# Performance work log

Measured on AMD Instinct MI355X. Metric: run time of the kernel, lower is better.

## Reference

```python
import jax, jax.numpy as jnp
import numpy as np


def setup_inputs() -> dict:
    key = jax.random.key(0)
    ks = jax.random.split(key, 6)
    B, S, D, U = 32, 2048, 1024, 1024
    scale = 1.0 / np.sqrt(D)
    return {
        "h_enc": jax.random.normal(ks[0], (B, S, D), dtype=jnp.float32),
        "h_dec": jax.random.normal(ks[1], (B, D), dtype=jnp.float32),
        "W_enc": jax.random.normal(ks[2], (D, U), dtype=jnp.float32) * scale,
        "b_enc": jnp.zeros((U,), dtype=jnp.float32),
        "W_dec": jax.random.normal(ks[3], (D, U), dtype=jnp.float32) * scale,
        "b_dec": jnp.zeros((U,), dtype=jnp.float32),
        "W_com": jax.random.normal(ks[4], (U, 1), dtype=jnp.float32) * (1.0 / np.sqrt(U)),
        "b_com": jnp.zeros((1,), dtype=jnp.float32),
    }


def reference(h_enc, h_dec, W_enc, b_enc, W_dec, b_dec, W_com, b_com):
    # h_enc: [B,S,D] -> projected enc features [B,S,U]
    enc_p = jnp.einsum("bsd,du->bsu", h_enc, W_enc) + b_enc
    # h_dec: [B,D] -> [B,1,U]
    dec_p = (h_dec @ W_dec + b_dec)[:, None, :]
    # additive score: [B,S,1]
    score = jnp.einsum("bsu,uo->bso", jnp.tanh(dec_p + enc_p), W_com) + b_com
    attn = jax.nn.softmax(score, axis=1)  # softmax over seq axis
    # NOTE: original code multiplies attn by the PROJECTED h_enc (reassigned)
    context_vec = jnp.sum(attn * enc_p, axis=1)  # [B,U]
    return (context_vec, attn)
```

## Files before the change

### kernel.cpp

```cpp
#include <hip/hip_runtime.h>
#include <math.h>
#include <stdint.h>

#define Bz 32
#define Sz 2048
#define Dz 1024
#define Uz 1024
#define Mz (Bz*Sz)

typedef __attribute__((ext_vector_type(8))) short bf16x8;
typedef __attribute__((ext_vector_type(4))) float f32x4;

__device__ __forceinline__ unsigned short f2bf(float f) {
    union { float f; uint32_t u; } v; v.f = f;
    uint32_t r = v.u + 0x7FFFu + ((v.u >> 16) & 1u);
    return (unsigned short)(r >> 16);
}

__device__ __forceinline__ float fast_tanh(float x) {
    float e = __expf(2.f * x);
    return 1.f - 2.f * __builtin_amdgcn_rcpf(e + 1.f);
}

#define GLD16(gsrc, ldst) \
    __builtin_amdgcn_global_load_lds((__attribute__((address_space(1))) void*)(void*)(gsrc), \
        (__attribute__((address_space(3))) void*)(ldst), 16, 0, 0)

#define CONV_BLOCKS 16384
#define WT_BLOCKS   256
#define DECI_BLOCKS 32
#define SINIT_BLOCKS 64

__global__ __launch_bounds__(256) void prep_kernel(
    const float* __restrict__ h_enc, unsigned short* __restrict__ hbf,
    const float* __restrict__ W_enc, unsigned short* __restrict__ wT,
    const float* __restrict__ b_dec, float* __restrict__ dec_p,
    const float* __restrict__ b_com, float* __restrict__ score)
{
    __shared__ float tile[64][65];
    const int bid = blockIdx.x;
    const int tid = threadIdx.x;
    if (bid < CONV_BLOCKS) {
        const size_t i = ((size_t)bid * 256 + tid) * 16;
#pragma unroll
        for (int h = 0; h < 2; ++h) {
            const float4 a = *(const float4*)(h_enc + i + h * 8);
            const float4 c = *(const float4*)(h_enc + i + h * 8 + 4);
            union { unsigned short s[8]; uint4 v; } o;
            o.s[0] = f2bf(a.x); o.s[1] = f2bf(a.y); o.s[2] = f2bf(a.z); o.s[3] = f2bf(a.w);
            o.s[4] = f2bf(c.x); o.s[5] = f2bf(c.y); o.s[6] = f2bf(c.z); o.s[7] = f2bf(c.w);
            *(uint4*)(hbf + i + h * 8) = o.v;
        }
    } else if (bid < CONV_BLOCKS + WT_BLOCKS) {
        const int b2 = bid - CONV_BLOCKS;
        const int c  = tid & 63;
        const int r0 = tid >> 6;
        const int u0 = (b2 & 15) * 64;
        const int d0 = (b2 >> 4) * 64;
        for (int r = r0; r < 64; r += 4)
            tile[r][c] = W_enc[(size_t)(d0 + r) * Uz + u0 + c];
        __syncthreads();
        for (int r = r0; r < 64; r += 4)
            wT[(size_t)(u0 + r) * Dz + d0 + c] = f2bf(tile[c][r]);
    } else if (bid < CONV_BLOCKS + WT_BLOCKS + DECI_BLOCKS) {
        const int b3 = bid - (CONV_BLOCKS + WT_BLOCKS);
        const int u4 = tid * 4;
        *(float4*)&dec_p[b3 * Uz + u4] = *(const float4*)&b_dec[u4];
    } else {
        const int b4 = bid - (CONV_BLOCKS + WT_BLOCKS + DECI_BLOCKS);
        const float bc = b_com[0];
        const int i4 = (b4 * 256 + tid) * 4;
        float4 v = {bc, bc, bc, bc};
        *(float4*)&score[i4] = v;
    }
}

__global__ __launch_bounds__(256) void dec_partial_kernel(
    const float* __restrict__ h_dec, const float* __restrict__ W_dec,
    float* __restrict__ dec_p)
{
    __shared__ float hs[128];
    const int b  = blockIdx.x >> 3;
    const int d0 = (blockIdx.x & 7) * 128;
    const int tid = threadIdx.x;
    const int u4 = tid * 4;
    if (tid < 128) hs[tid] = h_dec[b * Dz + d0 + tid];
    __syncthreads();
    float4 acc = {0.f, 0.f, 0.f, 0.f};
#pragma unroll 4
    for (int d = 0; d < 128; ++d) {
        const float  a = hs[d];
        const float4 w = *(const float4*)&W_dec[(size_t)(d0 + d) * Uz + u4];
        acc.x += a * w.x; acc.y += a * w.y; acc.z += a * w.z; acc.w += a * w.w;
    }
    float* o = dec_p + b * Uz + u4;
    atomicAdd(o + 0, acc.x); atomicAdd(o + 1, acc.y);
    atomicAdd(o + 2, acc.z); atomicAdd(o + 3, acc.w);
}

__global__ __launch_bounds__(512, 2) void score_mfma_kernel(
    const unsigned short* __restrict__ hbf,
    const unsigned short* __restrict__ wT,
    const float* __restrict__ dec_p,
    const float* __restrict__ W_com,
    float* __restrict__ score)
{
    __shared__ unsigned short As[2][32 * 512];
    __shared__ unsigned short Bs[2][32 * 512];
    __shared__ float sred[4][256];

    const int tid  = threadIdx.x;
    const int w    = tid >> 6;
    const int lane = tid & 63;
    const int ln   = lane & 15;
    const int q    = lane >> 4;
    const int wm   = w >> 2;
    const int wn   = w & 3;

    const int xcd = blockIdx.x & 7;
    const int idx = blockIdx.x >> 3;
    const int mb  = xcd * 32 + (idx >> 2);
    const int m0  = mb * 256;
    const int ub  = (idx & 3) * 256;
    const int b   = m0 / Sz;

    const unsigned short* aA0 = hbf + (size_t)(m0 + w * 32 + ln) * Dz + q * 8;
    const unsigned short* aA1 = aA0 + (size_t)16 * Dz;
    const unsigned short* bB0 = wT + (size_t)(ub + w * 32 + ln) * Dz + q * 8;
    const unsigned short* bB1 = bB0 + (size_t)16 * Dz;

#define STAGE(nb_, k0_) do { \
        unsigned short* ad = &As[nb_][(w * 4) * 512]; \
        unsigned short* bd = &Bs[nb_][(w * 4) * 512]; \
        GLD16(aA0 + (k0_),      ad); \
        GLD16(aA0 + (k0_) + 32, ad + 512); \
        GLD16(aA1 + (k0_),      ad + 1024); \
        GLD16(aA1 + (k0_) + 32, ad + 1536); \
        GLD16(bB0 + (k0_),      bd); \
        GLD16(bB0 + (k0_) + 32, bd + 512); \
        GLD16(bB1 + (k0_),      bd + 1024); \
        GLD16(bB1 + (k0_) + 32, bd + 1536); \
    } while (0)

    f32x4 acc[8][4];
#pragma unroll
    for (int i = 0; i < 8; ++i)
#pragma unroll
        for (int j = 0; j < 4; ++j) acc[i][j] = (f32x4){0.f, 0.f, 0.f, 0.f};

#define COMPUTE(cb_) do { \
        _Pragma("unroll") \
        for (int kh = 0; kh < 2; ++kh) { \
            bf16x8 af[8], bfr[4]; \
            _Pragma("unroll") \
            for (int i = 0; i < 8; ++i) \
                af[i] = *(const bf16x8*)(&As[cb_][(((wm * 8 + i) << 1) + kh) * 512 + lane * 8]); \
            _Pragma("unroll") \
            for (int j = 0; j < 4; ++j) \
                bfr[j] = *(const bf16x8*)(&Bs[cb_][(((wn * 4 + j) << 1) + kh) * 512 + lane * 8]); \
            _Pragma("unroll") \
            for (int i = 0; i < 8; ++i) \
                _Pragma("unroll") \
                for (int j = 0; j < 4; ++j) \
                    acc[i][j] = __builtin_amdgcn_mfma_f32_16x16x32_bf16( \
                        af[i], bfr[j], acc[i][j], 0, 0, 0); \
        } \
    } while (0)

    STAGE(0, 0);
    __syncthreads();

    int nb = 0;
    for (int t = 0; t < 15; ++t) {
        STAGE(nb ^ 1, (t + 1) * 64);
        COMPUTE(nb);
        __syncthreads();
        nb ^= 1;
    }
    COMPUTE(nb);

    float dpv[4], wcv[4];
#pragma unroll
    for (int j = 0; j < 4; ++j) {
        const int u = ub + wn * 64 + j * 16 + ln;
        dpv[j] = dec_p[b * Uz + u];
        wcv[j] = W_com[u];
    }
    float racc[8][4];
#pragma unroll
    for (int i = 0; i < 8; ++i)
#pragma unroll
        for (int r = 0; r < 4; ++r) {
            float v = 0.f;
#pragma unroll
            for (int j = 0; j < 4; ++j)
                v += fast_tanh(acc[i][j][r] + dpv[j]) * wcv[j];
            racc[i][r] = v;
        }
#pragma unroll
    for (int off = 1; off < 16; off <<= 1)
#pragma unroll
        for (int i = 0; i < 8; ++i)
#pragma unroll
            for (int r = 0; r < 4; ++r)
                racc[i][r] += __shfl_xor(racc[i][r], off, 64);
    if (ln == 0) {
#pragma unroll
        for (int i = 0; i < 8; ++i)
#pragma unroll
            for (int r = 0; r < 4; ++r)
                sred[wn][wm * 128 + i * 16 + q * 4 + r] = racc[i][r];
    }
    __syncthreads();
    if (tid < 256) {
        const float s = sred[0][tid] + sred[1][tid] + sred[2][tid] + sred[3][tid];
        atomicAdd(&score[m0 + tid], s);
    }
#undef STAGE
#undef COMPUTE
}

__global__ __launch_bounds__(256) void softmax_init_kernel(
    const float* __restrict__ score, float* __restrict__ attn,
    const float* __restrict__ b_enc, float* __restrict__ out_ctx,
    float* __restrict__ wsum)
{
    __shared__ float red[256];
    const int tid = threadIdx.x;
    if (blockIdx.x >= 2 * Bz) {
        const int b3 = blockIdx.x - 2 * Bz;
        float4 z = {0.f, 0.f, 0.f, 0.f};
        *(float4*)&wsum[b3 * Dz + tid * 4] = z;
        return;
    }
    if (blockIdx.x >= Bz) {
        const int b2 = blockIdx.x - Bz;
        const int u4 = tid * 4;
        *(float4*)&out_ctx[b2 * Uz + u4] = *(const float4*)&b_enc[u4];
        return;
    }
    const int b = blockIdx.x;
    const float* srow = score + b * Sz;
    float v[8];
    float lm = -1e30f;
#pragma unroll
    for (int i = 0; i < 8; ++i) { v[i] = srow[i * 256 + tid]; lm = fmaxf(lm, v[i]); }
    red[tid] = lm; __syncthreads();
    for (int off = 128; off > 0; off >>= 1) {
        if (tid < off) red[tid] = fmaxf(red[tid], red[tid + off]);
        __syncthreads();
    }
    const float mx = red[0];
    __syncthreads();
    float ls = 0.f;
#pragma unroll
    for (int i = 0; i < 8; ++i) { v[i] = expf(v[i] - mx); ls += v[i]; }
    red[tid] = ls; __syncthreads();
    for (int off = 128; off > 0; off >>= 1) {
        if (tid < off) red[tid] += red[tid + off];
        __syncthreads();
    }
    const float inv = 1.f / red[0];
#pragma unroll
    for (int i = 0; i < 8; ++i) attn[b * Sz + i * 256 + tid] = v[i] * inv;
}

__global__ __launch_bounds__(256) void wsum_kernel(
    const float* __restrict__ h_enc, const float* __restrict__ attn,
    float* __restrict__ wsum)
{
    __shared__ float aw[64];
    const int b  = blockIdx.x >> 5;
    const int s0 = (blockIdx.x & 31) * 64;
    const int tid = threadIdx.x;
    if (tid < 64) aw[tid] = attn[b * Sz + s0 + tid];
    __syncthreads();
    float4 acc = {0.f, 0.f, 0.f, 0.f};
    const float* base = h_enc + ((size_t)b * Sz + s0) * Dz + tid * 4;
#pragma unroll 4
    for (int s = 0; s < 64; ++s) {
        const float a = aw[s];
        const float4 h = *(const float4*)(base + (size_t)s * Dz);
        acc.x += a * h.x; acc.y += a * h.y; acc.z += a * h.z; acc.w += a * h.w;
    }
    float* o = wsum + b * Dz + tid * 4;
    atomicAdd(o + 0, acc.x); atomicAdd(o + 1, acc.y);
    atomicAdd(o + 2, acc.z); atomicAdd(o + 3, acc.w);
}

__global__ __launch_bounds__(256) void ctx_partial_kernel(
    const float* __restrict__ wsum, const float* __restrict__ W_enc,
    float* __restrict__ out_ctx)
{
    __shared__ float hs[128];
    const int b  = blockIdx.x >> 3;
    const int d0 = (blockIdx.x & 7) * 128;
    const int tid = threadIdx.x;
    const int u4 = tid * 4;
    if (tid < 128) hs[tid] = wsum[b * Dz + d0 + tid];
    __syncthreads();
    float4 acc = {0.f, 0.f, 0.f, 0.f};
#pragma unroll 4
    for (int d = 0; d < 128; ++d) {
        const float  a = hs[d];
        const float4 wv = *(const float4*)&W_enc[(size_t)(d0 + d) * Uz + u4];
        acc.x += a * wv.x; acc.y += a * wv.y; acc.z += a * wv.z; acc.w += a * wv.w;
    }
    float* o = out_ctx + b * Uz + u4;
    atomicAdd(o + 0, acc.x); atomicAdd(o + 1, acc.y);
    atomicAdd(o + 2, acc.z); atomicAdd(o + 3, acc.w);
}

__global__ __launch_bounds__(256) void dec_proj_kernel(
    const float* __restrict__ h_dec, const float* __restrict__ W_dec,
    const float* __restrict__ b_dec, float* __restrict__ dec_p)
{
    __shared__ float hs[Dz];
    const int b = blockIdx.x >> 2;
    const int u = ((blockIdx.x & 3) << 8) + threadIdx.x;
    for (int d = threadIdx.x; d < Dz; d += 256) hs[d] = h_dec[b * Dz + d];
    __syncthreads();
    float acc = 0.f;
#pragma unroll 4
    for (int d = 0; d < Dz; ++d) acc += hs[d] * W_dec[d * Uz + u];
    dec_p[b * Uz + u] = acc + b_dec[u];
}

#define MT 64
#define NT 64
#define KT 64
__global__ __launch_bounds__(256) void score_kernel(
    const float* __restrict__ h_enc, const float* __restrict__ W_enc,
    const float* __restrict__ dec_p, const float* __restrict__ W_com,
    const float* __restrict__ b_com, float* __restrict__ score)
{
    __shared__ __align__(16) float As[KT][MT + 4];
    __shared__ __align__(16) float Bs[KT][NT + 4];
    __shared__ float red[MT][17];
    const int tid = threadIdx.x;
    const int tx = tid & 15;
    const int ty = tid >> 4;
    const int m0 = blockIdx.x * MT;
    const int b  = m0 / Sz;
    float s_acc = 0.f;
    for (int u0 = 0; u0 < Uz; u0 += NT) {
        float acc[4][4];
#pragma unroll
        for (int i = 0; i < 4; ++i)
#pragma unroll
            for (int j = 0; j < 4; ++j) acc[i][j] = 0.f;
        for (int k0 = 0; k0 < Dz; k0 += KT) {
            __syncthreads();
#pragma unroll
            for (int i = 0; i < 4; ++i) {
                const int row = ty + i * 16;
                const int c4  = tx * 4;
                const float4 v = *(const float4*)&h_enc[(size_t)(m0 + row) * Dz + k0 + c4];
                As[c4 + 0][row] = v.x; As[c4 + 1][row] = v.y;
                As[c4 + 2][row] = v.z; As[c4 + 3][row] = v.w;
            }
#pragma unroll
            for (int i = 0; i < 4; ++i) {
                const int row = ty + i * 16;
                *(float4*)&Bs[row][tx * 4] =
                    *(const float4*)&W_enc[(size_t)(k0 + row) * Uz + u0 + tx * 4];
            }
            __syncthreads();
#pragma unroll 8
            for (int k = 0; k < KT; ++k) {
                const float4 a = *(const float4*)&As[k][ty * 4];
                const float4 wv = *(const float4*)&Bs[k][tx * 4];
                acc[0][0] += a.x * wv.x; acc[0][1] += a.x * wv.y; acc[0][2] += a.x * wv.z; acc[0][3] += a.x * wv.w;
                acc[1][0] += a.y * wv.x; acc[1][1] += a.y * wv.y; acc[1][2] += a.y * wv.z; acc[1][3] += a.y * wv.w;
                acc[2][0] += a.z * wv.x; acc[2][1] += a.z * wv.y; acc[2][2] += a.z * wv.z; acc[2][3] += a.z * wv.w;
                acc[3][0] += a.w * wv.x; acc[3][1] += a.w * wv.y; acc[3][2] += a.w * wv.z; acc[3][3] += a.w * wv.w;
            }
        }
        const float4 dp = *(const float4*)&dec_p[b * Uz + u0 + tx * 4];
        const float4 wc = *(const float4*)&W_com[u0 + tx * 4];
#pragma unroll
        for (int i = 0; i < 4; ++i) {
            const float p = tanhf(acc[i][0] + dp.x) * wc.x + tanhf(acc[i][1] + dp.y) * wc.y
                          + tanhf(acc[i][2] + dp.z) * wc.z + tanhf(acc[i][3] + dp.w) * wc.w;
            red[ty * 4 + i][tx] = p;
        }
        __syncthreads();
        if (tid < MT) {
            float t = 0.f;
#pragma unroll
            for (int j = 0; j < 16; ++j) t += red[tid][j];
            s_acc += t;
        }
    }
    if (tid < MT) score[m0 + tid] = s_acc + b_com[0];
}

__global__ __launch_bounds__(256) void ctx_kernel(
    const float* __restrict__ wsum, const float* __restrict__ W_enc,
    const float* __restrict__ b_enc, float* __restrict__ out)
{
    __shared__ float hs[Dz];
    const int b = blockIdx.x >> 2;
    const int u = ((blockIdx.x & 3) << 8) + threadIdx.x;
    for (int d = threadIdx.x; d < Dz; d += 256) hs[d] = wsum[b * Dz + d];
    __syncthreads();
    float acc = 0.f;
#pragma unroll 4
    for (int d = 0; d < Dz; ++d) acc += hs[d] * W_enc[d * Uz + u];
    out[b * Uz + u] = acc + b_enc[u];
}

extern "C" void kernel_launch(void* const* d_in, const int* in_sizes, int n_in,
                              void* d_out, int out_size, void* d_ws, size_t ws_size,
                              hipStream_t stream)
{
    const float* h_enc = (const float*)d_in[0];
    const float* h_dec = (const float*)d_in[1];
    const float* W_enc = (const float*)d_in[2];
    const float* b_enc = (const float*)d_in[3];
    const float* W_dec = (const float*)d_in[4];
    const float* b_dec = (const float*)d_in[5];
    const float* W_com = (const float*)d_in[6];
    const float* b_com = (const float*)d_in[7];

    float* out_ctx  = (float*)d_out;
    float* out_attn = out_ctx + Bz * Uz;

    const size_t HBF_BYTES = (size_t)Mz * Dz * 2;
    const size_t WT_BYTES  = (size_t)Uz * Dz * 2;
    const size_t SMALL     = (size_t)(Bz*Uz + Bz*Sz + Bz*Dz) * 4;
    const size_t need      = HBF_BYTES + WT_BYTES + SMALL;

    if (ws_size >= need) {
        char* wsb = (char*)d_ws;
        unsigned short* hbf = (unsigned short*)wsb;
        unsigned short* wT  = (unsigned short*)(wsb + HBF_BYTES);
        float* dec_p = (float*)(wsb + HBF_BYTES + WT_BYTES);
        float* score = dec_p + Bz * Uz;
        float* wsum  = score + Bz * Sz;

        prep_kernel<<<CONV_BLOCKS + WT_BLOCKS + DECI_BLOCKS + SINIT_BLOCKS, 256, 0, stream>>>(
            h_enc, hbf, W_enc, wT, b_dec, dec_p, b_com, score);
        dec_partial_kernel<<<Bz * 8, 256, 0, stream>>>(h_dec, W_dec, dec_p);
        score_mfma_kernel<<<(Mz / 256) * (Uz / 256), 512, 0, stream>>>(hbf, wT, dec_p, W_com, score);
        softmax_init_kernel<<<3 * Bz, 256, 0, stream>>>(score, out_attn, b_enc, out_ctx, wsum);
        wsum_kernel<<<Bz * 32, 256, 0, stream>>>(h_enc, out_attn, wsum);
        ctx_partial_kernel<<<Bz * 8, 256, 0, stream>>>(wsum, W_enc, out_ctx);
    } else {
        float* ws    = (float*)d_ws;
        float* dec_p = ws;
        float* score = ws + Bz * Uz;
        float* wsum  = ws + Bz * Uz + Bz * Sz;

        dec_proj_kernel<<<(Bz * Uz) / 256, 256, 0, stream>>>(h_dec, W_dec, b_dec, dec_p);
        score_kernel<<<Mz / MT, 256, 0, stream>>>(h_enc, W_enc, dec_p, W_com, b_com, score);
        softmax_init_kernel<<<3 * Bz, 256, 0, stream>>>(score, out_attn, b_enc, out_ctx, wsum);
        wsum_kernel<<<Bz * 32, 256, 0, stream>>>(h_enc, out_attn, wsum);
        ctx_kernel<<<(Bz * Uz) / 256, 256, 0, stream>>>(wsum, W_enc, b_enc, out_ctx);
    }
}
```

Measured before the change: 705.1 us.

## Restructure score GEMM main loop into 4-stage half-tile pipeline with ping-pong scheduling

Replaces the double-buffered 64-wide K loop with a 4-slot ring of 32-wide K slices, keeping three slices of global-to-LDS loads in flight. Each iteration is split into two MFMA phases interleaved with LDS reads, loads into the next slot, explicit vmcnt/lgkmcnt waits and workgroup barriers. s_setprio raises priority around the MFMA blocks, in the style of 8-wave ping-pong schedules. The aim is to hide global load latency and overlap LDS reads with matrix math, at the cost of more barriers per K step and fragile hand-counted waitcnt logic.

```diff
diff --git a/kernel.cpp b/kernel.cpp
--- a/kernel.cpp
+++ b/kernel.cpp
@@ -105,8 +105,7 @@
     const float* __restrict__ W_com,
     float* __restrict__ score)
 {
-    __shared__ unsigned short As[2][32 * 512];
-    __shared__ unsigned short Bs[2][32 * 512];
+    __shared__ unsigned short LB[4][32][512];
     __shared__ float sred[4][256];
 
     const int tid  = threadIdx.x;
@@ -129,55 +128,83 @@
     const unsigned short* bB0 = wT + (size_t)(ub + w * 32 + ln) * Dz + q * 8;
     const unsigned short* bB1 = bB0 + (size_t)16 * Dz;
 
-#define STAGE(nb_, k0_) do { \
-        unsigned short* ad = &As[nb_][(w * 4) * 512]; \
-        unsigned short* bd = &Bs[nb_][(w * 4) * 512]; \
-        GLD16(aA0 + (k0_),      ad); \
-        GLD16(aA0 + (k0_) + 32, ad + 512); \
-        GLD16(aA1 + (k0_),      ad + 1024); \
-        GLD16(aA1 + (k0_) + 32, ad + 1536); \
-        GLD16(bB0 + (k0_),      bd); \
-        GLD16(bB0 + (k0_) + 32, bd + 512); \
-        GLD16(bB1 + (k0_),      bd + 1024); \
-        GLD16(bB1 + (k0_) + 32, bd + 1536); \
-    } while (0)
-
     f32x4 acc[8][4];
 #pragma unroll
     for (int i = 0; i < 8; ++i)
 #pragma unroll
         for (int j = 0; j < 4; ++j) acc[i][j] = (f32x4){0.f, 0.f, 0.f, 0.f};
 
-#define COMPUTE(cb_) do { \
-        _Pragma("unroll") \
-        for (int kh = 0; kh < 2; ++kh) { \
-            bf16x8 af[8], bfr[4]; \
-            _Pragma("unroll") \
-            for (int i = 0; i < 8; ++i) \
-                af[i] = *(const bf16x8*)(&As[cb_][(((wm * 8 + i) << 1) + kh) * 512 + lane * 8]); \
-            _Pragma("unroll") \
-            for (int j = 0; j < 4; ++j) \
-                bfr[j] = *(const bf16x8*)(&Bs[cb_][(((wn * 4 + j) << 1) + kh) * 512 + lane * 8]); \
-            _Pragma("unroll") \
-            for (int i = 0; i < 8; ++i) \
-                _Pragma("unroll") \
-                for (int j = 0; j < 4; ++j) \
-                    acc[i][j] = __builtin_amdgcn_mfma_f32_16x16x32_bf16( \
-                        af[i], bfr[j], acc[i][j], 0, 0, 0); \
-        } \
-    } while (0)
-
-    STAGE(0, 0);
-    __syncthreads();
-
-    int nb = 0;
-    for (int t = 0; t < 15; ++t) {
-        STAGE(nb ^ 1, (t + 1) * 64);
-        COMPUTE(nb);
-        __syncthreads();
-        nb ^= 1;
-    }
-    COMPUTE(nb);
+#pragma unroll
+    for (int h = 0; h < 3; ++h) {
+        const int K = (h >> 1) * 64 + (h & 1) * 32;
+        GLD16(aA0 + K, &LB[h][2 * w][0]);
+        GLD16(aA1 + K, &LB[h][2 * w + 1][0]);
+        GLD16(bB0 + K, &LB[h][16 + 2 * w][0]);
+        GLD16(bB1 + K, &LB[h][16 + 2 * w + 1][0]);
+    }
+    asm volatile("s_waitcnt vmcnt(8)" ::: "memory");
+    __builtin_amdgcn_s_barrier();
+    __builtin_amdgcn_sched_barrier(0);
+
+    for (int H = 0; H < 32; ++H) {
+        const int sl = H & 3;
+        const int h3 = H + 3;
+        const int s3 = h3 & 3;
+        const int K3 = (h3 >> 1) * 64 + (h3 & 1) * 32;
+        bf16x8 af[4], bfr[4];
+
+#pragma unroll
+        for (int i = 0; i < 4; ++i)
+            af[i] = *(const bf16x8*)&LB[sl][wm * 8 + i][lane * 8];
+#pragma unroll
+        for (int j = 0; j < 4; ++j)
+            bfr[j] = *(const bf16x8*)&LB[sl][16 + wn * 4 + j][lane * 8];
+        if (h3 < 32) {
+            GLD16(aA0 + K3, &LB[s3][2 * w][0]);
+            GLD16(aA1 + K3, &LB[s3][2 * w + 1][0]);
+        }
+        __builtin_amdgcn_sched_barrier(0);
+        __builtin_amdgcn_s_barrier();
+        asm volatile("s_waitcnt lgkmcnt(0)" ::: "memory");
+        __builtin_amdgcn_sched_barrier(0);
+        __builtin_amdgcn_s_setprio(1);
+#pragma unroll
+        for (int i = 0; i < 4; ++i)
+#pragma unroll
+            for (int j = 0; j < 4; ++j)
+                acc[i][j] = __builtin_amdgcn_mfma_f32_16x16x32_bf16(
+                    af[i], bfr[j], acc[i][j], 0, 0, 0);
+        __builtin_amdgcn_s_setprio(0);
+        __builtin_amdgcn_sched_barrier(0);
+        __builtin_amdgcn_s_barrier();
+        __builtin_amdgcn_sched_barrier(0);
+
+#pragma unroll
+        for (int i = 0; i < 4; ++i)
+            af[i] = *(const bf16x8*)&LB[sl][wm * 8 + 4 + i][lane * 8];
+        if (h3 < 32) {
+            GLD16(bB0 + K3, &LB[s3][16 + 2 * w][0]);
+            GLD16(bB1 + K3, &LB[s3][16 + 2 * w + 1][0]);
+        }
+        if (H < 29)       { asm volatile("s_waitcnt vmcnt(8)" ::: "memory"); }
+        else if (H == 29) { asm volatile("s_waitcnt vmcnt(4)" ::: "memory"); }
+        else if (H == 30) { asm volatile("s_waitcnt vmcnt(0)" ::: "memory"); }
+        __builtin_amdgcn_sched_barrier(0);
+        __builtin_amdgcn_s_barrier();
+        asm volatile("s_waitcnt lgkmcnt(0)" ::: "memory");
+        __builtin_amdgcn_sched_barrier(0);
+        __builtin_amdgcn_s_setprio(1);
+#pragma unroll
+        for (int i = 0; i < 4; ++i)
+#pragma unroll
+            for (int j = 0; j < 4; ++j)
+                acc[4 + i][j] = __builtin_amdgcn_mfma_f32_16x16x32_bf16(
+                    af[i], bfr[j], acc[4 + i][j], 0, 0, 0);
+        __builtin_amdgcn_s_setprio(0);
+        __builtin_amdgcn_sched_barrier(0);
+        __builtin_amdgcn_s_barrier();
+        __builtin_amdgcn_sched_barrier(0);
+    }
 
     float dpv[4], wcv[4];
 #pragma unroll
@@ -216,8 +243,6 @@
         const float s = sred[0][tid] + sred[1][tid] + sred[2][tid] + sred[3][tid];
         atomicAdd(&score[m0 + tid], s);
     }
-#undef STAGE
-#undef COMPUTE
 }
 
 __global__ __launch_bounds__(256) void softmax_init_kernel(
```

Measured after the change: 668.5 us. 5.2% less time.
